# Performance work log

Hardware: AMD Instinct MI355X
Metric: run time of the kernel (lower is better)

## Reference

```python
import jax, jax.numpy as jnp
import numpy as np
from itertools import combinations

# NOTE: the original embed_vec_sort references `q` (inf-masking) even when
# varying_set_size=False, where q is undefined (a latent bug / NameError path).
# Both embeddings here are constructed with varying_set_size=False, so the
# intended math is the plain sort-embedding without masking, implemented below.

def _embed_vec_sort(X, A, w):
    # X: [b, d, n], A: [d, d_out], w: [1, n, d_out] -> out: [b, d_out]
    prod = jnp.einsum('bdn,de->ben', X, A)                     # [b, d_out, n]
    prod_sort = jnp.sort(prod, axis=2)                         # sort along set dim
    return jnp.sum(prod_sort * jnp.transpose(w, (0, 2, 1)), axis=2)


def setup_inputs() -> dict:
    key = jax.random.key(0)
    b, d, n = 4, 3, 48
    de = d                      # d + d_feature, d_feature = 0
    ne = n - (d - 1)            # 46
    d_out_comb = 2 * de * ne + 1            # 277
    n_combs = n * (n - 1)                   # 2256
    d_comb = d * d + 2 * de * ne + 1        # 286
    d_graph = 2 * de * n + 1                # 289
    k1, k2, k3, k4, k5 = jax.random.split(key, 5)
    return {
        'x': jax.random.normal(k1, (b, d, n), jnp.float32),
        'A_comb': jax.random.normal(k2, (de, d_out_comb), jnp.float32),
        'w_comb': jax.random.normal(k3, (1, ne, d_out_comb), jnp.float32),
        'A_graph': jax.random.normal(k4, (d_comb, d_graph), jnp.float32),
        'w_graph': jax.random.normal(k5, (1, n_combs, d_graph), jnp.float32),
    }


def reference(x, A_comb, w_comb, A_graph, w_graph):
    b, d, n = x.shape            # d == 3
    # translation invariance: subtract centroid
    X = x - jnp.mean(x, axis=2, keepdims=True)

    # static index sets: all ordered pairs (combinations then flipped)
    pairs = np.array(list(combinations(range(n), 2)), dtype=np.int32)   # [n(n-1)/2, 2]
    combs = np.concatenate([pairs, pairs[:, ::-1]], axis=0)             # [C, 2]
    C = combs.shape[0]
    all_idx = np.arange(n)
    combcomp = np.stack([np.setdiff1d(all_idx, c) for c in combs])      # [C, n-2], sorted

    Xc = X[:, :, combs]                                                 # [b, 3, C, 2]
    xprod = jnp.cross(Xc[:, :, :, 0], Xc[:, :, :, 1], axis=1)          # [b, 3, C]
    M = jnp.concatenate([Xc, xprod[:, :, :, None]], axis=3)            # [b, 3, C, 3]

    MtM = jnp.einsum('bjck,bjcl->bckl', M, M)                          # [b, C, 3, 3]
    vec1 = MtM.reshape(b, C, 9)                                        # row-major flatten

    Xcomp = X[:, :, combcomp]                                          # [b, 3, C, n-2]
    MtV = jnp.einsum('bjck,bjcm->bckm', M, Xcomp)                      # [b, C, 3, n-2]
    ne = n - 2
    vec2 = _embed_vec_sort(MtV.reshape(b * C, 3, ne), A_comb, w_comb)  # [b*C, d_out_comb]
    vec2 = vec2.reshape(b, C, -1)

    global_vecs = jnp.concatenate([vec1, vec2], axis=2)                # [b, C, d_comb]
    global_vecs = jnp.transpose(global_vecs, (0, 2, 1))                # [b, d_comb, C]
    return _embed_vec_sort(global_vecs, A_graph, w_graph)              # [b, d_graph]
```

## Files before the change

kernel.cpp:

```cpp
#include <hip/hip_runtime.h>
#include <float.h>

#define N_PTS   48
#define N_PAIRS 1128
#define C_TOT   2256
#define NE      46
#define DOC     277
#define DCOMB   286
#define GSTRIDE 288
#define DGRAPH  289
#define BATCH   4

typedef _Float16 h2 __attribute__((ext_vector_type(2)));


__global__ void center_kernel(const float* __restrict__ x, float* __restrict__ xc) {
    int row = blockIdx.x;
    int t = threadIdx.x;
    float v = (t < N_PTS) ? x[row * N_PTS + t] : 0.f;
    float s = v;
    #pragma unroll
    for (int m = 32; m >= 1; m >>= 1) s += __shfl_xor(s, m);
    if (t < N_PTS) xc[row * N_PTS + t] = v - s * (1.0f / N_PTS);
}

__global__ __launch_bounds__(256) void transpose_tiled(const float* __restrict__ in,
                                                       float* __restrict__ out, int R, int C) {
    __shared__ float tile[32][33];
    int r0 = blockIdx.x * 32, c0 = blockIdx.y * 32;
    int tx = threadIdx.x & 31, ty = threadIdx.x >> 5;
    #pragma unroll
    for (int yy = 0; yy < 4; yy++) {
        int r = r0 + ty + 8 * yy, c = c0 + tx;
        tile[ty + 8 * yy][tx] = (r < R && c < C) ? in[r * C + c] : 0.f;
    }
    __syncthreads();
    #pragma unroll
    for (int yy = 0; yy < 4; yy++) {
        int c = c0 + ty + 8 * yy, r = r0 + tx;
        if (c < C && r < R) out[(size_t)c * R + r] = tile[tx][ty + 8 * yy];
    }
}


__device__ __forceinline__ void batcher46h2(h2 a[NE]) {
    #pragma unroll
    for (int p = 1; p < 64; p <<= 1) {
        #pragma unroll
        for (int k = p; k >= 1; k >>= 1) {
            #pragma unroll
            for (int j = k % p; j + k < 64; j += 2 * k) {
                #pragma unroll
                for (int i = 0; i < k; i++) {
                    int lo = i + j, hi = i + j + k;
                    if (hi < NE && (lo / (2 * p)) == (hi / (2 * p))) {
                        h2 mn = __builtin_elementwise_min(a[lo], a[hi]);
                        h2 mx = __builtin_elementwise_max(a[lo], a[hi]);
                        a[lo] = mn; a[hi] = mx;
                    }
                }
            }
        }
    }
}

__device__ __forceinline__ void decode_pair(int c, int& fi, int& se, int& pi, int& pj) {
    int cc = c % N_PAIRS;
    bool rev = c >= N_PAIRS;
    int i = 0, rem = cc;
    while (rem >= N_PTS - 1 - i) { rem -= N_PTS - 1 - i; i++; }
    int j = i + 1 + rem;
    pi = i; pj = j;
    fi = rev ? j : i; se = rev ? i : j;
}

__device__ __forceinline__ void pick_row(int k, float x0, float y0, float z0,
                                         float x1, float y1, float z1,
                                         float x2, float y2, float z2,
                                         float& u0, float& u1, float& u2) {
    u0 = (k == 0) ? x0 : (k == 1) ? x1 : x2;
    u1 = (k == 0) ? y0 : (k == 1) ? y1 : y2;
    u2 = (k == 0) ? z0 : (k == 1) ? z1 : z2;
}

__device__ __forceinline__ void sort2_dot(int e, const float* __restrict__ A_comb,
                                          const float* __restrict__ w_comb,
                                          const h2 (*MtVp)[NE],
                                          float* __restrict__ dst0,
                                          float* __restrict__ dst1) {
    float A0 = A_comb[e], A1 = A_comb[DOC + e], A2 = A_comb[2 * DOC + e];
    h2 A0p = { (_Float16)A0, (_Float16)A0 };
    h2 A1p = { (_Float16)A1, (_Float16)A1 };
    h2 A2p = { (_Float16)A2, (_Float16)A2 };
    h2 p[NE];
    #pragma unroll
    for (int n = 0; n < NE; n++)
        p[n] = A0p * MtVp[0][n] + A1p * MtVp[1][n] + A2p * MtVp[2][n];
    batcher46h2(p);
    float acc0 = 0.f, acc1 = 0.f;
    #pragma unroll
    for (int n = 0; n < NE; n++) {
        float w = w_comb[n * DOC + e];
        acc0 += (float)p[n].x * w;
        acc1 += (float)p[n].y * w;
    }
    dst0[9 + e] = acc0;
    dst1[9 + e] = acc1;
}

__global__ __launch_bounds__(256) void pair_kernel(
        const float* __restrict__ xc, const float* __restrict__ A_comb,
        const float* __restrict__ w_comb, float* __restrict__ gvR) {
    int blk = blockIdx.x;
    int b = blk / N_PAIRS, k = blk % N_PAIRS;
    int c0 = 2 * k, c1 = 2 * k + 1;
    int tid = threadIdx.x;

    __shared__ float Xs[3][N_PTS];
    __shared__ float MtVf[2][3][NE];
    __shared__ h2 MtVp[3][NE];

    if (tid < 3 * N_PTS) ((float*)Xs)[tid] = xc[b * 3 * N_PTS + tid];
    __syncthreads();

    int f0, s0, i0, j0; decode_pair(c0, f0, s0, i0, j0);
    int f1, s1, i1, j1; decode_pair(c1, f1, s1, i1, j1);

    float ax0 = Xs[0][f0], ay0 = Xs[1][f0], az0 = Xs[2][f0];
    float bx0 = Xs[0][s0], by0 = Xs[1][s0], bz0 = Xs[2][s0];
    float cx0 = ay0 * bz0 - az0 * by0;
    float cy0 = az0 * bx0 - ax0 * bz0;
    float cz0 = ax0 * by0 - ay0 * bx0;

    float ax1 = Xs[0][f1], ay1 = Xs[1][f1], az1 = Xs[2][f1];
    float bx1 = Xs[0][s1], by1 = Xs[1][s1], bz1 = Xs[2][s1];
    float cx1 = ay1 * bz1 - az1 * by1;
    float cy1 = az1 * bx1 - ax1 * bz1;
    float cz1 = ax1 * by1 - ay1 * bx1;

    float* dst0 = gvR + ((size_t)b * C_TOT + c0) * GSTRIDE;
    float* dst1 = gvR + ((size_t)b * C_TOT + c1) * GSTRIDE;

    if (tid < NE) {
        int m = tid;
        int a = (m < i0) ? m : m + 1;
        a = (a < j0) ? a : a + 1;
        float v0 = Xs[0][a], v1 = Xs[1][a], v2 = Xs[2][a];
        MtVf[0][0][m] = ax0 * v0 + ay0 * v1 + az0 * v2;
        MtVf[0][1][m] = bx0 * v0 + by0 * v1 + bz0 * v2;
        MtVf[0][2][m] = cx0 * v0 + cy0 * v1 + cz0 * v2;
    } else if (tid >= 64 && tid < 64 + NE) {
        int m = tid - 64;
        int a = (m < i1) ? m : m + 1;
        a = (a < j1) ? a : a + 1;
        float v0 = Xs[0][a], v1 = Xs[1][a], v2 = Xs[2][a];
        MtVf[1][0][m] = ax1 * v0 + ay1 * v1 + az1 * v2;
        MtVf[1][1][m] = bx1 * v0 + by1 * v1 + bz1 * v2;
        MtVf[1][2][m] = cx1 * v0 + cy1 * v1 + cz1 * v2;
    }

    if (tid >= 160 && tid < 169) {
        int q = tid - 160, kk = q / 3, ll = q % 3;
        float u0, u1, u2, v0, v1, v2;
        pick_row(kk, ax0, ay0, az0, bx0, by0, bz0, cx0, cy0, cz0, u0, u1, u2);
        pick_row(ll, ax0, ay0, az0, bx0, by0, bz0, cx0, cy0, cz0, v0, v1, v2);
        dst0[q] = u0 * v0 + u1 * v1 + u2 * v2;
    }
    if (tid >= 192 && tid < 201) {
        int q = tid - 192, kk = q / 3, ll = q % 3;
        float u0, u1, u2, v0, v1, v2;
        pick_row(kk, ax1, ay1, az1, bx1, by1, bz1, cx1, cy1, cz1, u0, u1, u2);
        pick_row(ll, ax1, ay1, az1, bx1, by1, bz1, cx1, cy1, cz1, v0, v1, v2);
        dst1[q] = u0 * v0 + u1 * v1 + u2 * v2;
    }
    if (tid == 224) { dst0[DCOMB] = 0.f; dst0[DCOMB + 1] = 0.f; }
    if (tid == 225) { dst1[DCOMB] = 0.f; dst1[DCOMB + 1] = 0.f; }
    __syncthreads();

    if (tid < 3 * NE) {
        int d = tid / NE, n = tid % NE;
        h2 t; t.x = (_Float16)MtVf[0][d][n]; t.y = (_Float16)MtVf[1][d][n];
        MtVp[d][n] = t;
    }
    __syncthreads();

    sort2_dot(tid, A_comb, w_comb, MtVp, dst0, dst1);
    if (tid < DOC - 256)
        sort2_dot(256 + tid, A_comb, w_comb, MtVp, dst0, dst1);
}

#define KT 32

__global__ __launch_bounds__(256) void proj_gemm(
        const float* __restrict__ gvR, const float* __restrict__ A_graph,
        float* __restrict__ P) {
    __shared__ __align__(16) float As[KT][64];
    __shared__ __align__(16) float Gs[KT][68];
    int b = blockIdx.z;
    int e0 = blockIdx.y * 64;
    int c0 = blockIdx.x * 64;
    int tid = threadIdx.x;
    int tx = tid & 15, ty = tid >> 4;
    float acc[4][4] = {};
    const float* gbase = gvR + (size_t)b * C_TOT * GSTRIDE;

    for (int k0 = 0; k0 < GSTRIDE; k0 += KT) {
        #pragma unroll
        for (int o = 0; o < 8; o++) {
            int idx = o * 256 + tid;
            int kk = idx >> 6, ee = idx & 63;
            int k = k0 + kk, E = e0 + ee;
            As[kk][ee] = (k < DCOMB && E < DGRAPH) ? A_graph[k * DGRAPH + E] : 0.f;
        }
        int kk = tid & 31;
        int cb = tid >> 5;
        #pragma unroll
        for (int o = 0; o < 8; o++) {
            int ccol = o * 8 + cb;
            int C = c0 + ccol;
            Gs[kk][ccol] = (C < C_TOT) ? gbase[(size_t)C * GSTRIDE + k0 + kk] : 0.f;
        }
        __syncthreads();
        #pragma unroll
        for (int k = 0; k < KT; k++) {
            float4 av = *(const float4*)&As[k][ty * 4];
            float4 gq = *(const float4*)&Gs[k][tx * 4];
            float ar[4] = {av.x, av.y, av.z, av.w};
            float gr[4] = {gq.x, gq.y, gq.z, gq.w};
            #pragma unroll
            for (int ii = 0; ii < 4; ii++)
                #pragma unroll
                for (int jj = 0; jj < 4; jj++)
                    acc[ii][jj] += ar[ii] * gr[jj];
        }
        __syncthreads();
    }
    #pragma unroll
    for (int ii = 0; ii < 4; ii++) {
        int e = e0 + ty * 4 + ii;
        int c = c0 + tx * 4;
        if (e < DGRAPH && c < C_TOT) {
            float4 val = make_float4(acc[ii][0], acc[ii][1], acc[ii][2], acc[ii][3]);
            *(float4*)&P[((size_t)b * DGRAPH + e) * C_TOT + c] = val;
        }
    }
}


#define RPT 16
#define LSTRIDE 17

template<int J, int K>
__device__ __forceinline__ void bpass_in(float v[RPT], int tid) {
    bool upt = ((tid & (K >> 4)) == 0);
    #pragma unroll
    for (int r = 0; r < RPT; r++) {
        int l = r ^ J;
        if (l > r) {
            bool up = (K < 16) ? ((r & K) == 0) : upt;
            float a = v[r], b = v[l];
            float mn = fminf(a, b), mx = fmaxf(a, b);
            v[r] = up ? mn : mx;
            v[l] = up ? mx : mn;
        }
    }
}

template<int JL, int K>
__device__ __forceinline__ void bpass_shfl(float v[RPT], int tid) {
    bool lower = (tid & JL) == 0;
    bool up = (tid & (K >> 4)) == 0;
    bool keep_min = (lower == up);
    #pragma unroll
    for (int r = 0; r < RPT; r++) {
        float pv = __shfl_xor(v[r], JL);
        float mn = fminf(v[r], pv), mx = fmaxf(v[r], pv);
        v[r] = keep_min ? mn : mx;
    }
}

template<int JL, int K>
__device__ __forceinline__ void bpass_lds(float v[RPT], int tid, float* lds) {
    __syncthreads();
    #pragma unroll
    for (int r = 0; r < RPT; r++) lds[tid * LSTRIDE + r] = v[r];
    __syncthreads();
    bool lower = (tid & JL) == 0;
    bool up = (tid & (K >> 4)) == 0;
    bool keep_min = (lower == up);
    int pbase = (tid ^ JL) * LSTRIDE;
    #pragma unroll
    for (int r = 0; r < RPT; r++) {
        float pv = lds[pbase + r];
        float mn = fminf(v[r], pv), mx = fmaxf(v[r], pv);
        v[r] = keep_min ? mn : mx;
    }
}

#define BIN4(K) bpass_in<8,K>(v,tid); bpass_in<4,K>(v,tid); \
                bpass_in<2,K>(v,tid); bpass_in<1,K>(v,tid)

__global__ __launch_bounds__(256) void sort_kernel(
        const float* __restrict__ P, const float* __restrict__ wgT,
        float* __restrict__ out) {
    int blk = blockIdx.x;
    int b = blk / DGRAPH, e = blk % DGRAPH;
    int tid = threadIdx.x;
    __shared__ float lds[256 * LSTRIDE];
    __shared__ float red[4];

    float v[RPT];
    const float* row = P + ((size_t)b * DGRAPH + e) * C_TOT;
    if (tid < 141) {
        const float4* r4 = (const float4*)(row + tid * RPT);
        #pragma unroll
        for (int q = 0; q < 4; q++) {
            float4 tq = r4[q];
            v[q * 4 + 0] = tq.x; v[q * 4 + 1] = tq.y;
            v[q * 4 + 2] = tq.z; v[q * 4 + 3] = tq.w;
        }
    } else {
        #pragma unroll
        for (int r = 0; r < RPT; r++) v[r] = FLT_MAX;
    }

    bpass_in<1,2>(v,tid);
    bpass_in<2,4>(v,tid); bpass_in<1,4>(v,tid);
    bpass_in<4,8>(v,tid); bpass_in<2,8>(v,tid); bpass_in<1,8>(v,tid);
    bpass_in<8,16>(v,tid); bpass_in<4,16>(v,tid); bpass_in<2,16>(v,tid); bpass_in<1,16>(v,tid);
    bpass_shfl<1,32>(v,tid);  BIN4(32);
    bpass_shfl<2,64>(v,tid);  bpass_shfl<1,64>(v,tid);  BIN4(64);
    bpass_shfl<4,128>(v,tid); bpass_shfl<2,128>(v,tid); bpass_shfl<1,128>(v,tid); BIN4(128);
    bpass_shfl<8,256>(v,tid); bpass_shfl<4,256>(v,tid); bpass_shfl<2,256>(v,tid); bpass_shfl<1,256>(v,tid); BIN4(256);
    bpass_shfl<16,512>(v,tid); bpass_shfl<8,512>(v,tid); bpass_shfl<4,512>(v,tid); bpass_shfl<2,512>(v,tid); bpass_shfl<1,512>(v,tid); BIN4(512);
    bpass_shfl<32,1024>(v,tid); bpass_shfl<16,1024>(v,tid); bpass_shfl<8,1024>(v,tid); bpass_shfl<4,1024>(v,tid); bpass_shfl<2,1024>(v,tid); bpass_shfl<1,1024>(v,tid); BIN4(1024);
    bpass_lds<64,2048>(v,tid,lds);
    bpass_shfl<32,2048>(v,tid); bpass_shfl<16,2048>(v,tid); bpass_shfl<8,2048>(v,tid); bpass_shfl<4,2048>(v,tid); bpass_shfl<2,2048>(v,tid); bpass_shfl<1,2048>(v,tid); BIN4(2048);
    bpass_lds<128,4096>(v,tid,lds);
    bpass_lds<64,4096>(v,tid,lds);
    bpass_shfl<32,4096>(v,tid); bpass_shfl<16,4096>(v,tid); bpass_shfl<8,4096>(v,tid); bpass_shfl<4,4096>(v,tid); bpass_shfl<2,4096>(v,tid); bpass_shfl<1,4096>(v,tid); BIN4(4096);

    float acc = 0.f;
    if (tid < 141) {
        const float4* w4 = (const float4*)(wgT + (size_t)e * C_TOT + tid * RPT);
        #pragma unroll
        for (int q = 0; q < 4; q++) {
            float4 tq = w4[q];
            acc += v[q * 4 + 0] * tq.x + v[q * 4 + 1] * tq.y
                 + v[q * 4 + 2] * tq.z + v[q * 4 + 3] * tq.w;
        }
    }
    #pragma unroll
    for (int m = 32; m >= 1; m >>= 1) acc += __shfl_xor(acc, m);
    int wave = tid >> 6, lane = tid & 63;
    if (lane == 0) red[wave] = acc;
    __syncthreads();
    if (tid == 0) out[b * DGRAPH + e] = red[0] + red[1] + red[2] + red[3];
}


extern "C" void kernel_launch(void* const* d_in, const int* in_sizes, int n_in,
                              void* d_out, int out_size, void* d_ws, size_t ws_size,
                              hipStream_t stream) {
    const float* x       = (const float*)d_in[0];
    const float* A_comb  = (const float*)d_in[1];
    const float* w_comb  = (const float*)d_in[2];
    const float* A_graph = (const float*)d_in[3];
    const float* w_graph = (const float*)d_in[4];
    float* out = (float*)d_out;

    float* ws  = (float*)d_ws;
    float* xc  = ws;
    float* wgT = xc + 576;
    float* gvR = wgT + 651984;
    float* P   = gvR + 2598912;

    center_kernel<<<12, 64, 0, stream>>>(x, xc);
    transpose_tiled<<<dim3((C_TOT + 31) / 32, (DGRAPH + 31) / 32), 256, 0, stream>>>(
        w_graph, wgT, C_TOT, DGRAPH);
    pair_kernel<<<BATCH * N_PAIRS, 256, 0, stream>>>(xc, A_comb, w_comb, gvR);
    proj_gemm<<<dim3(36, 5, BATCH), 256, 0, stream>>>(gvR, A_graph, P);
    sort_kernel<<<BATCH * DGRAPH, 256, 0, stream>>>(P, wgT, out);
}
```

Before: 171.3 us.

## Store packed fp16 MtV directly and use 320 threads to cover all outputs in one pass

Pair kernel now writes MtV results straight into an interleaved fp16 shared buffer, which removes the float staging array, a repack step and one barrier. Block size grows from 256 to 320 so every one of the 277 output columns gets its own thread, avoiding a second serial sort pass for 21 threads. Shared reads use 16-byte h8 vectors to cut LDS instruction count. The cost is more threads per block, which may lower occupancy given the register-heavy 46-element sort.

```diff
diff --git a/kernel.cpp b/kernel.cpp
--- a/kernel.cpp
+++ b/kernel.cpp
@@ -12,6 +12,7 @@
 #define BATCH   4
 
 typedef _Float16 h2 __attribute__((ext_vector_type(2)));
+typedef _Float16 h8 __attribute__((ext_vector_type(8)));
 
 
 __global__ void center_kernel(const float* __restrict__ x, float* __restrict__ xc) {
@@ -83,32 +84,7 @@
     u2 = (k == 0) ? z0 : (k == 1) ? z1 : z2;
 }
 
-__device__ __forceinline__ void sort2_dot(int e, const float* __restrict__ A_comb,
-                                          const float* __restrict__ w_comb,
-                                          const h2 (*MtVp)[NE],
-                                          float* __restrict__ dst0,
-                                          float* __restrict__ dst1) {
-    float A0 = A_comb[e], A1 = A_comb[DOC + e], A2 = A_comb[2 * DOC + e];
-    h2 A0p = { (_Float16)A0, (_Float16)A0 };
-    h2 A1p = { (_Float16)A1, (_Float16)A1 };
-    h2 A2p = { (_Float16)A2, (_Float16)A2 };
-    h2 p[NE];
-    #pragma unroll
-    for (int n = 0; n < NE; n++)
-        p[n] = A0p * MtVp[0][n] + A1p * MtVp[1][n] + A2p * MtVp[2][n];
-    batcher46h2(p);
-    float acc0 = 0.f, acc1 = 0.f;
-    #pragma unroll
-    for (int n = 0; n < NE; n++) {
-        float w = w_comb[n * DOC + e];
-        acc0 += (float)p[n].x * w;
-        acc1 += (float)p[n].y * w;
-    }
-    dst0[9 + e] = acc0;
-    dst1[9 + e] = acc1;
-}
-
-__global__ __launch_bounds__(256) void pair_kernel(
+__global__ __launch_bounds__(320) void pair_kernel(
         const float* __restrict__ xc, const float* __restrict__ A_comb,
         const float* __restrict__ w_comb, float* __restrict__ gvR) {
     int blk = blockIdx.x;
@@ -117,8 +93,8 @@
     int tid = threadIdx.x;
 
     __shared__ float Xs[3][N_PTS];
-    __shared__ float MtVf[2][3][NE];
-    __shared__ h2 MtVp[3][NE];
+    __shared__ h8 MtVp8[3][12];
+    _Float16* MtVh = (_Float16*)MtVp8;
 
     if (tid < 3 * N_PTS) ((float*)Xs)[tid] = xc[b * 3 * N_PTS + tid];
     __syncthreads();
@@ -146,17 +122,21 @@
         int a = (m < i0) ? m : m + 1;
         a = (a < j0) ? a : a + 1;
         float v0 = Xs[0][a], v1 = Xs[1][a], v2 = Xs[2][a];
-        MtVf[0][0][m] = ax0 * v0 + ay0 * v1 + az0 * v2;
-        MtVf[0][1][m] = bx0 * v0 + by0 * v1 + bz0 * v2;
-        MtVf[0][2][m] = cx0 * v0 + cy0 * v1 + cz0 * v2;
+        MtVh[0 * 96 + m * 2] = (_Float16)(ax0 * v0 + ay0 * v1 + az0 * v2);
+        MtVh[1 * 96 + m * 2] = (_Float16)(bx0 * v0 + by0 * v1 + bz0 * v2);
+        MtVh[2 * 96 + m * 2] = (_Float16)(cx0 * v0 + cy0 * v1 + cz0 * v2);
     } else if (tid >= 64 && tid < 64 + NE) {
         int m = tid - 64;
         int a = (m < i1) ? m : m + 1;
         a = (a < j1) ? a : a + 1;
         float v0 = Xs[0][a], v1 = Xs[1][a], v2 = Xs[2][a];
-        MtVf[1][0][m] = ax1 * v0 + ay1 * v1 + az1 * v2;
-        MtVf[1][1][m] = bx1 * v0 + by1 * v1 + bz1 * v2;
-        MtVf[1][2][m] = cx1 * v0 + cy1 * v1 + cz1 * v2;
+        MtVh[0 * 96 + m * 2 + 1] = (_Float16)(ax1 * v0 + ay1 * v1 + az1 * v2);
+        MtVh[1 * 96 + m * 2 + 1] = (_Float16)(bx1 * v0 + by1 * v1 + bz1 * v2);
+        MtVh[2 * 96 + m * 2 + 1] = (_Float16)(cx1 * v0 + cy1 * v1 + cz1 * v2);
+    } else if (tid >= 128 && tid < 134) {
+        int q = tid - 128;
+        int d = q >> 1, n = 46 + (q & 1);
+        ((h2*)MtVp8)[d * 48 + n] = (h2){(_Float16)0.f, (_Float16)0.f};
     }
 
     if (tid >= 160 && tid < 169) {
@@ -177,16 +157,40 @@
     if (tid == 225) { dst1[DCOMB] = 0.f; dst1[DCOMB + 1] = 0.f; }
     __syncthreads();
 
-    if (tid < 3 * NE) {
-        int d = tid / NE, n = tid % NE;
-        h2 t; t.x = (_Float16)MtVf[0][d][n]; t.y = (_Float16)MtVf[1][d][n];
-        MtVp[d][n] = t;
-    }
-    __syncthreads();
-
-    sort2_dot(tid, A_comb, w_comb, MtVp, dst0, dst1);
-    if (tid < DOC - 256)
-        sort2_dot(256 + tid, A_comb, w_comb, MtVp, dst0, dst1);
+    if (tid < DOC) {
+        int e = tid;
+        float A0 = A_comb[e], A1 = A_comb[DOC + e], A2 = A_comb[2 * DOC + e];
+        h2 A0p = { (_Float16)A0, (_Float16)A0 };
+        h2 A1p = { (_Float16)A1, (_Float16)A1 };
+        h2 A2p = { (_Float16)A2, (_Float16)A2 };
+        h2 p[NE];
+        #pragma unroll
+        for (int c8 = 0; c8 < 12; c8++) {
+            h8 m0 = MtVp8[0][c8];
+            h8 m1 = MtVp8[1][c8];
+            h8 m2 = MtVp8[2][c8];
+            #pragma unroll
+            for (int q = 0; q < 4; q++) {
+                int n = c8 * 4 + q;
+                if (n < NE) {
+                    h2 w0 = { m0[2 * q], m0[2 * q + 1] };
+                    h2 w1 = { m1[2 * q], m1[2 * q + 1] };
+                    h2 w2 = { m2[2 * q], m2[2 * q + 1] };
+                    p[n] = A0p * w0 + A1p * w1 + A2p * w2;
+                }
+            }
+        }
+        batcher46h2(p);
+        float acc0 = 0.f, acc1 = 0.f;
+        #pragma unroll
+        for (int n = 0; n < NE; n++) {
+            float w = w_comb[n * DOC + e];
+            acc0 += (float)p[n].x * w;
+            acc1 += (float)p[n].y * w;
+        }
+        dst0[9 + e] = acc0;
+        dst1[9 + e] = acc1;
+    }
 }
 
 #define KT 32
@@ -378,7 +382,7 @@
     center_kernel<<<12, 64, 0, stream>>>(x, xc);
     transpose_tiled<<<dim3((C_TOT + 31) / 32, (DGRAPH + 31) / 32), 256, 0, stream>>>(
         w_graph, wgT, C_TOT, DGRAPH);
-    pair_kernel<<<BATCH * N_PAIRS, 256, 0, stream>>>(xc, A_comb, w_comb, gvR);
+    pair_kernel<<<BATCH * N_PAIRS, 320, 0, stream>>>(xc, A_comb, w_comb, gvR);
     proj_gemm<<<dim3(36, 5, BATCH), 256, 0, stream>>>(gvR, A_graph, P);
     sort_kernel<<<BATCH * DGRAPH, 256, 0, stream>>>(P, wgT, out);
 }
```

Result: faster. 153.8 us (-10.2%).
